# Kernel tuning notes

Hardware: AMD Instinct MI355X
Metric: run time of the kernel (lower is better)

The kernel has to match this reference:

```python
import jax, jax.numpy as jnp
import numpy as np

DT = 0.05
SQRT_DT = float(np.sqrt(DT))
MIN_V, MAX_V = -5.0, 5.0
B, FS, FA, T, H = 2048, 32, 16, 512, 64


def setup_inputs() -> dict:
    key = jax.random.key(0)
    ks = jax.random.split(key, 10)
    scale_f1 = 1.0 / np.sqrt(FA + FS)
    scale_2 = 1.0 / np.sqrt(H)
    return {
        "ts": jnp.arange(T, dtype=jnp.float32) * DT,
        "in_signal": jax.random.normal(ks[0], (B, FA, T), dtype=jnp.float32),
        "x0": jax.random.normal(ks[1], (B, FS), dtype=jnp.float32),
        "noise": jax.random.normal(ks[2], (T - 1, B, FS), dtype=jnp.float32),
        "Wf1": jax.random.normal(ks[3], (FA + FS, H), dtype=jnp.float32) * scale_f1,
        "bf1": jnp.zeros((H,), dtype=jnp.float32),
        "Wf2": jax.random.normal(ks[4], (H, FS), dtype=jnp.float32) * scale_2,
        "bf2": jnp.zeros((FS,), dtype=jnp.float32),
        "Wg1": jax.random.normal(ks[5], (FA + FS, H), dtype=jnp.float32) * scale_f1,
        "bg1": jnp.zeros((H,), dtype=jnp.float32),
        "Wg2": jax.random.normal(ks[6], (H, FS), dtype=jnp.float32) * scale_2,
        "bg2": jnp.zeros((FS,), dtype=jnp.float32),
    }


def _mlp(s, W1, b1, W2, b2):
    return jnp.tanh(s @ W1 + b1) @ W2 + b2


def reference(ts, in_signal, x0, noise, Wf1, bf1, Wf2, bf2, Wg1, bg1, Wg2, bg2):
    # in_signal: (B, FA, T); per-step action a_t = in_signal[..., n-1]
    a_seq = jnp.moveaxis(in_signal[..., : T - 1], -1, 0)  # (T-1, B, FA)

    def step(x_t, inp):
        a_t, eps = inp  # (B,FA), (B,FS)
        s = jnp.concatenate([a_t, x_t], axis=-1)  # g concat order: [in_signal, x0]
        drift = _mlp(s, Wf1, bf1, Wf2, bf2)
        diff = _mlp(s, Wg1, bg1, Wg2, bg2) * (eps * SQRT_DT)  # dW ~ N(0, dt)
        x_tp1 = jnp.clip(drift + diff, MIN_V, MAX_V)
        return x_tp1, x_tp1

    _, xs = jax.lax.scan(step, x0, (a_seq, noise))  # xs: (T-1, B, FS)
    out = jnp.concatenate([x0[None], xs], axis=0)  # (T, B, FS)
    return jnp.moveaxis(out, 0, -1).transpose(1, 0, 2)  # -> wrong; fixed below


def _check():
    pass


# Correct final layout: torch.stack(x_list, dim=-1) -> (B, FS, T)

def reference(ts, in_signal, x0, noise, Wf1, bf1, Wf2, bf2, Wg1, bg1, Wg2, bg2):
    a_seq = jnp.moveaxis(in_signal[..., : T - 1], -1, 0)  # (T-1, B, FA)

    def step(x_t, inp):
        a_t, eps = inp
        s = jnp.concatenate([a_t, x_t], axis=-1)
        drift = _mlp(s, Wf1, bf1, Wf2, bf2)
        diff = _mlp(s, Wg1, bg1, Wg2, bg2) * (eps * SQRT_DT)
        x_tp1 = jnp.clip(drift + diff, MIN_V, MAX_V)
        return x_tp1, x_tp1

    _, xs = jax.lax.scan(step, x0, (a_seq, noise))
    out = jnp.concatenate([x0[None], xs], axis=0)  # (T, B, FS)
    return jnp.transpose(out, (1, 2, 0))  # (B, FS, T)
```

## Files before the change

kernel.cpp:

```cpp
#include <hip/hip_runtime.h>


#define SQRT_DT_F 0.22360679774997896f

typedef float v2f __attribute__((ext_vector_type(2)));
typedef float v4f __attribute__((ext_vector_type(4)));

#define PK(acc, s, w) (acc) = __builtin_elementwise_fma((s), (w), (acc))

__device__ __forceinline__ float fast_tanh(float y) {
    float e = __expf(2.0f * y);
    return 1.0f - 2.0f / (e + 1.0f);
}

__device__ __forceinline__ void wave_sync() {
    __builtin_amdgcn_fence(__ATOMIC_SEQ_CST, "wavefront");
    __builtin_amdgcn_sched_barrier(0x047F);
}

__global__ __launch_bounds__(64, 2)
void sde_kernel(const float* __restrict__ in_signal,
                const float* __restrict__ x0v,
                const float* __restrict__ noise,
                const float* __restrict__ Wf1, const float* __restrict__ bf1,
                const float* __restrict__ Wf2, const float* __restrict__ bf2,
                const float* __restrict__ Wg1, const float* __restrict__ bg1,
                const float* __restrict__ Wg2, const float* __restrict__ bg2,
                float* __restrict__ out)
{
    const int lane = threadIdx.x;
    const int b    = blockIdx.x;

    __shared__ __align__(16) float hbuf[2][128];
    __shared__ __align__(16) float xbuf[32];
    __shared__ __align__(16) float abuf[2][4][16];

    v2f w1fv[24], w1gv[24];
#pragma unroll
    for (int k2 = 0; k2 < 24; ++k2) {
        w1fv[k2] = v2f{Wf1[(2 * k2) * 64 + lane], Wf1[(2 * k2 + 1) * 64 + lane]};
        w1gv[k2] = v2f{Wg1[(2 * k2) * 64 + lane], Wg1[(2 * k2 + 1) * 64 + lane]};
    }
    v2f w2v[32];
    const float* W2p = (lane < 32) ? (Wf2 + lane) : (Wg2 + (lane - 32));
#pragma unroll
    for (int g = 0; g < 8; ++g)
#pragma unroll
        for (int i = 0; i < 4; ++i)
            w2v[g * 4 + i] = v2f{W2p[(8 * g + i) * 32], W2p[(8 * g + 4 + i) * 32]};

    const float b1f = bf1[lane];
    const float b1g = bg1[lane];
    const float b2  = (lane < 32) ? bf2[lane] : bg2[lane - 32];

    float x_cur = x0v[b * 32 + (lane & 31)];
    if (lane < 32) xbuf[lane] = x_cur;
    float xq[4];
    xq[0] = x_cur;

    const int sig = (lane & ~7) | ((lane & 3) << 1) | ((lane >> 2) & 1);
    float* hw0 = &hbuf[0][sig];
    float* hw1 = &hbuf[1][sig];
    const float* hsrc0 = hbuf[0] + ((lane >> 5) << 6);
    const float* hsrc1 = hbuf[1] + ((lane >> 5) << 6);
    const float* a_base = in_signal + ((size_t)(b * 16 + (lane & 15)) << 9);
    const float* noise_lane = noise + (size_t)b * 32 + (lane & 31);
    float* out_ptr = out + ((size_t)b * 32 + (lane & 31)) * 512;

    float eps_c = noise_lane[0];
    float eps_n = noise_lane[65536];

    {
        float4 a0 = *(const float4*)(a_base);
        if (lane < 16) {
            abuf[0][0][lane] = a0.x;
            abuf[0][1][lane] = a0.y;
            abuf[0][2][lane] = a0.z;
            abuf[0][3][lane] = a0.w;
        }
    }
    wave_sync();

#define STEP(tt) do {                                                           \
    const int t_ = tq4 + (tt);                                                  \
                     \
    int tf_ = t_ + 2; if (tf_ > 510) tf_ = 510;                                 \
    float eps_f = noise_lane[(size_t)tf_ << 16];                                \
             \
    v4f sq[12];                                                                 \
    sq[0] = *(const v4f*)&ab_[tt][0];                                           \
    sq[1] = *(const v4f*)&ab_[tt][4];                                           \
    sq[2] = *(const v4f*)&ab_[tt][8];                                           \
    sq[3] = *(const v4f*)&ab_[tt][12];                                          \
    _Pragma("unroll")                                                           \
    for (int q = 0; q < 8; ++q)                                                 \
        sq[4 + q] = *(const v4f*)&xbuf[q * 4];                                  \
       \
    v2f af = v2f{b1f, 0.f}, ag = v2f{b1g, 0.f};                                 \
    _Pragma("unroll")                                                           \
    for (int q = 0; q < 12; ++q) {                                              \
        v2f slo = sq[q].xy, shi = sq[q].zw;                                     \
        PK(af, slo, w1fv[2 * q]);                                               \
        PK(ag, slo, w1gv[2 * q]);                                               \
        PK(af, shi, w1fv[2 * q + 1]);                                           \
        PK(ag, shi, w1gv[2 * q + 1]);                                           \
    }                                                                           \
    float hfv = fast_tanh(af.x + af.y);                                         \
    float hgv = fast_tanh(ag.x + ag.y);                                         \
    {          \
        float* hw_ = ((tt) & 1) ? hw1 : hw0;                                    \
        hw_[0]  = hfv;                                                          \
        hw_[64] = hgv;                                                          \
    }                                                                           \
    wave_sync();                                                                \
             \
    {                                                                           \
        const float* hs_ = ((tt) & 1) ? hsrc1 : hsrc0;                          \
        v2f a2 = v2f{b2, 0.f};          \
        _Pragma("unroll")                                                       \
        for (int g = 0; g < 8; ++g) {                                           \
            const v4f qa = *(const v4f*)&hs_[g * 8];                            \
            const v4f qb = *(const v4f*)&hs_[g * 8 + 4];                        \
            v2f p0 = qa.xy, p1 = qa.zw, p2 = qb.xy, p3 = qb.zw;                 \
            PK(a2, p0, w2v[g * 4 + 0]);                                         \
            PK(a2, p1, w2v[g * 4 + 1]);                                         \
            PK(a2, p2, w2v[g * 4 + 2]);                                         \
            PK(a2, p3, w2v[g * 4 + 3]);                                         \
        }                                                                       \
        float acc2 = a2.x + a2.y;                                               \
        float other = __shfl_xor(acc2, 32, 64);                                 \
        float drift = (lane < 32) ? acc2 : other;                               \
        float gpre  = (lane < 32) ? other : acc2;                               \
        float xi = fmaf(gpre, eps_c * SQRT_DT_F, drift);                        \
        xi = fminf(5.0f, fmaxf(-5.0f, xi));                                     \
        x_cur = xi;                                                             \
        if (lane < 32) xbuf[lane] = xi;                                         \
        xq[((tt) + 1) & 3] = xi;                                                \
        if ((tt) == 2) {                                                        \
            if (lane < 32)                                                      \
                *(float4*)(out_ptr + tq4) =                                     \
                    make_float4(xq[0], xq[1], xq[2], xq[3]);                    \
        }                                                                       \
    }                                                                           \
    wave_sync();                                                                \
    eps_c = eps_n; eps_n = eps_f;                                               \
} while (0)

    for (int tq = 0; tq < 127; ++tq) {
        const int tq4 = tq * 4;
        const float (*ab_)[16] = abuf[tq & 1];
        float4 aq_n = *(const float4*)(a_base + tq4 + 4);
        STEP(0);
        if (lane < 16) {
            float (*abn)[16] = abuf[(tq + 1) & 1];
            abn[0][lane] = aq_n.x;
            abn[1][lane] = aq_n.y;
            abn[2][lane] = aq_n.z;
            abn[3][lane] = aq_n.w;
        }
        STEP(1); STEP(2); STEP(3);
    }
    {
        const int tq4 = 508;
        const float (*ab_)[16] = abuf[127 & 1];
        STEP(0); STEP(1); STEP(2);
    }
#undef STEP
}

extern "C" void kernel_launch(void* const* d_in, const int* in_sizes, int n_in,
                              void* d_out, int out_size, void* d_ws, size_t ws_size,
                              hipStream_t stream) {
    const float* in_signal = (const float*)d_in[1];
    const float* x0v   = (const float*)d_in[2];
    const float* noise = (const float*)d_in[3];
    const float* Wf1 = (const float*)d_in[4];
    const float* bf1 = (const float*)d_in[5];
    const float* Wf2 = (const float*)d_in[6];
    const float* bf2 = (const float*)d_in[7];
    const float* Wg1 = (const float*)d_in[8];
    const float* bg1 = (const float*)d_in[9];
    const float* Wg2 = (const float*)d_in[10];
    const float* bg2 = (const float*)d_in[11];
    float* out = (float*)d_out;

    hipLaunchKernelGGL(sde_kernel, dim3(2048), dim3(64), 0, stream,
                       in_signal, x0v, noise, Wf1, bf1, Wf2, bf2,
                       Wg1, bg1, Wg2, bg2, out);
}
```

Measured before the change: 588.3 us.

## Split drift and diffusion MLPs across two wavefronts per block

Each block now runs two wavefronts. One computes the drift MLP and the other the diffusion MLP, and they exchange the drift result through LDS behind a block barrier. This halves the per-wave layer-1 work and register footprint and doubles the wave count, trading the previous single-wave fence-only sync for two s_barriers per timestep. The serial recurrence latency now includes barrier costs, and half the lanes of the second layer sit idle.

```diff
diff --git a/kernel.cpp b/kernel.cpp
--- a/kernel.cpp
+++ b/kernel.cpp
@@ -18,7 +18,14 @@
     __builtin_amdgcn_sched_barrier(0x047F);
 }
 
-__global__ __launch_bounds__(64, 2)
+__device__ __forceinline__ void block_sync_lds() {
+    asm volatile("s_waitcnt lgkmcnt(0)" ::: "memory");
+    __builtin_amdgcn_sched_barrier(0);
+    __builtin_amdgcn_s_barrier();
+    __builtin_amdgcn_sched_barrier(0);
+}
+
+__global__ __launch_bounds__(128, 2)
 void sde_kernel(const float* __restrict__ in_signal,
                 const float* __restrict__ x0v,
                 const float* __restrict__ noise,
@@ -28,49 +35,55 @@
                 const float* __restrict__ Wg2, const float* __restrict__ bg2,
                 float* __restrict__ out)
 {
-    const int lane = threadIdx.x;
-    const int b    = blockIdx.x;
+    const int tid    = threadIdx.x;
+    const int wid    = tid >> 6;
+    const int lane   = tid & 63;
+    const int lane31 = lane & 31;
+    const int b      = blockIdx.x;
 
-    __shared__ __align__(16) float hbuf[2][128];
+    __shared__ __align__(16) float hbuf[2][64];
     __shared__ __align__(16) float xbuf[32];
     __shared__ __align__(16) float abuf[2][4][16];
+    __shared__ __align__(16) float dbuf[32];
 
-    v2f w1fv[24], w1gv[24];
+    const float* W1 = wid ? Wg1 : Wf1;
+    const float* B1 = wid ? bg1 : bf1;
+    const float* W2 = wid ? Wg2 : Wf2;
+    const float* B2 = wid ? bg2 : bf2;
+
+    v2f w1v[24];
 #pragma unroll
-    for (int k2 = 0; k2 < 24; ++k2) {
-        w1fv[k2] = v2f{Wf1[(2 * k2) * 64 + lane], Wf1[(2 * k2 + 1) * 64 + lane]};
-        w1gv[k2] = v2f{Wg1[(2 * k2) * 64 + lane], Wg1[(2 * k2 + 1) * 64 + lane]};
-    }
+    for (int k2 = 0; k2 < 24; ++k2)
+        w1v[k2] = v2f{W1[(2 * k2) * 64 + lane], W1[(2 * k2 + 1) * 64 + lane]};
     v2f w2v[32];
-    const float* W2p = (lane < 32) ? (Wf2 + lane) : (Wg2 + (lane - 32));
+    const float* W2p = W2 + lane31;
 #pragma unroll
     for (int g = 0; g < 8; ++g)
 #pragma unroll
         for (int i = 0; i < 4; ++i)
             w2v[g * 4 + i] = v2f{W2p[(8 * g + i) * 32], W2p[(8 * g + 4 + i) * 32]};
 
-    const float b1f = bf1[lane];
-    const float b1g = bg1[lane];
-    const float b2  = (lane < 32) ? bf2[lane] : bg2[lane - 32];
-
-    float x_cur = x0v[b * 32 + (lane & 31)];
-    if (lane < 32) xbuf[lane] = x_cur;
-    float xq[4];
-    xq[0] = x_cur;
+    const float b1 = B1[lane];
+    const float b2 = B2[lane31];
 
     const int sig = (lane & ~7) | ((lane & 3) << 1) | ((lane >> 2) & 1);
-    float* hw0 = &hbuf[0][sig];
-    float* hw1 = &hbuf[1][sig];
-    const float* hsrc0 = hbuf[0] + ((lane >> 5) << 6);
-    const float* hsrc1 = hbuf[1] + ((lane >> 5) << 6);
+    float* hw_ = &hbuf[wid][sig];
+    const float* hs_ = hbuf[wid];
+
     const float* a_base = in_signal + ((size_t)(b * 16 + (lane & 15)) << 9);
-    const float* noise_lane = noise + (size_t)b * 32 + (lane & 31);
-    float* out_ptr = out + ((size_t)b * 32 + (lane & 31)) * 512;
+    const float* noise_lane = noise + (size_t)b * 32 + lane31;
+    float* out_ptr = out + ((size_t)b * 32 + lane31) * 512;
 
-    float eps_c = noise_lane[0];
-    float eps_n = noise_lane[65536];
+    float eps_c = 0.f, eps_n = 0.f;
+    float xq[4] = {0.f, 0.f, 0.f, 0.f};
 
-    {
+    if (wid) {
+        eps_c = noise_lane[0];
+        eps_n = noise_lane[65536];
+        float x_init = x0v[b * 32 + lane31];
+        xbuf[lane31] = x_init;
+        xq[0] = x_init;
+    } else {
         float4 a0 = *(const float4*)(a_base);
         if (lane < 16) {
             abuf[0][0][lane] = a0.x;
@@ -79,13 +92,13 @@
             abuf[0][3][lane] = a0.w;
         }
     }
-    wave_sync();
+    block_sync_lds();
 
 #define STEP(tt) do {                                                           \
-    const int t_ = tq4 + (tt);                                                  \
-                     \
-    int tf_ = t_ + 2; if (tf_ > 510) tf_ = 510;                                 \
-    float eps_f = noise_lane[(size_t)tf_ << 16];                                \
+                 \
+    int tf_ = tq4 + (tt) + 2; if (tf_ > 510) tf_ = 510;                         \
+    float eps_f = 0.f;                                                          \
+    if (wid) eps_f = noise_lane[(size_t)tf_ << 16];                             \
              \
     v4f sq[12];                                                                 \
     sq[0] = *(const v4f*)&ab_[tt][0];                                           \
@@ -95,46 +108,37 @@
     _Pragma("unroll")                                                           \
     for (int q = 0; q < 8; ++q)                                                 \
         sq[4 + q] = *(const v4f*)&xbuf[q * 4];                                  \
-       \
-    v2f af = v2f{b1f, 0.f}, ag = v2f{b1g, 0.f};                                 \
+     \
+    v2f a1 = v2f{b1, 0.f};                                                      \
     _Pragma("unroll")                                                           \
     for (int q = 0; q < 12; ++q) {                                              \
         v2f slo = sq[q].xy, shi = sq[q].zw;                                     \
-        PK(af, slo, w1fv[2 * q]);                                               \
-        PK(ag, slo, w1gv[2 * q]);                                               \
-        PK(af, shi, w1fv[2 * q + 1]);                                           \
-        PK(ag, shi, w1gv[2 * q + 1]);                                           \
+        PK(a1, slo, w1v[2 * q]);                                                \
+        PK(a1, shi, w1v[2 * q + 1]);                                            \
     }                                                                           \
-    float hfv = fast_tanh(af.x + af.y);                                         \
-    float hgv = fast_tanh(ag.x + ag.y);                                         \
-    {          \
-        float* hw_ = ((tt) & 1) ? hw1 : hw0;                                    \
-        hw_[0]  = hfv;                                                          \
-        hw_[64] = hgv;                                                          \
+    float hv = fast_tanh(a1.x + a1.y);                                          \
+    hw_[0] = hv;                                                                \
+    wave_sync();                        \
+            \
+    v2f a2 = v2f{b2, 0.f};                                                      \
+    _Pragma("unroll")                                                           \
+    for (int g = 0; g < 8; ++g) {                                               \
+        const v4f qa = *(const v4f*)&hs_[g * 8];                                \
+        const v4f qb = *(const v4f*)&hs_[g * 8 + 4];                            \
+        v2f p0 = qa.xy, p1 = qa.zw, p2 = qb.xy, p3 = qb.zw;                     \
+        PK(a2, p0, w2v[g * 4 + 0]);                                             \
+        PK(a2, p1, w2v[g * 4 + 1]);                                             \
+        PK(a2, p2, w2v[g * 4 + 2]);                                             \
+        PK(a2, p3, w2v[g * 4 + 3]);                                             \
     }                                                                           \
-    wave_sync();                                                                \
-             \
-    {                                                                           \
-        const float* hs_ = ((tt) & 1) ? hsrc1 : hsrc0;                          \
-        v2f a2 = v2f{b2, 0.f};          \
-        _Pragma("unroll")                                                       \
-        for (int g = 0; g < 8; ++g) {                                           \
-            const v4f qa = *(const v4f*)&hs_[g * 8];                            \
-            const v4f qb = *(const v4f*)&hs_[g * 8 + 4];                        \
-            v2f p0 = qa.xy, p1 = qa.zw, p2 = qb.xy, p3 = qb.zw;                 \
-            PK(a2, p0, w2v[g * 4 + 0]);                                         \
-            PK(a2, p1, w2v[g * 4 + 1]);                                         \
-            PK(a2, p2, w2v[g * 4 + 2]);                                         \
-            PK(a2, p3, w2v[g * 4 + 3]);                                         \
-        }                                                                       \
-        float acc2 = a2.x + a2.y;                                               \
-        float other = __shfl_xor(acc2, 32, 64);                                 \
-        float drift = (lane < 32) ? acc2 : other;                               \
-        float gpre  = (lane < 32) ? other : acc2;                               \
-        float xi = fmaf(gpre, eps_c * SQRT_DT_F, drift);                        \
+    float res = a2.x + a2.y;                         \
+    if (!wid) dbuf[lane31] = res;                   \
+    block_sync_lds();                        \
+    if (wid) {                                                                  \
+        float drift = dbuf[lane31];                                             \
+        float xi = fmaf(res, eps_c * SQRT_DT_F, drift);                         \
         xi = fminf(5.0f, fmaxf(-5.0f, xi));                                     \
-        x_cur = xi;                                                             \
-        if (lane < 32) xbuf[lane] = xi;                                         \
+        xbuf[lane31] = xi;                          \
         xq[((tt) + 1) & 3] = xi;                                                \
         if ((tt) == 2) {                                                        \
             if (lane < 32)                                                      \
@@ -142,16 +146,17 @@
                     make_float4(xq[0], xq[1], xq[2], xq[3]);                    \
         }                                                                       \
     }                                                                           \
-    wave_sync();                                                                \
+    block_sync_lds();                     \
     eps_c = eps_n; eps_n = eps_f;                                               \
 } while (0)
 
     for (int tq = 0; tq < 127; ++tq) {
         const int tq4 = tq * 4;
         const float (*ab_)[16] = abuf[tq & 1];
-        float4 aq_n = *(const float4*)(a_base + tq4 + 4);
+        float4 aq_n;
+        if (!wid) aq_n = *(const float4*)(a_base + tq4 + 4);
         STEP(0);
-        if (lane < 16) {
+        if (!wid && lane < 16) {
             float (*abn)[16] = abuf[(tq + 1) & 1];
             abn[0][lane] = aq_n.x;
             abn[1][lane] = aq_n.y;
@@ -184,7 +189,7 @@
     const float* bg2 = (const float*)d_in[11];
     float* out = (float*)d_out;
 
-    hipLaunchKernelGGL(sde_kernel, dim3(2048), dim3(64), 0, stream,
+    hipLaunchKernelGGL(sde_kernel, dim3(2048), dim3(128), 0, stream,
                        in_signal, x0v, noise, Wf1, bf1, Wf2, bf2,
                        Wg1, bg1, Wg2, bg2, out);
 }
```

Result: slower. 1.111 ms (+88.9%).
